# Kernel tuning notes

Measured on AMD Instinct MI355X. Metric: run time of the kernel, lower is better.

The kernel has to match this reference:

```python
import jax, jax.numpy as jnp
import numpy as np

NT, NTRACES, NCH = 4096, 1024, 4


def setup_inputs() -> dict:
    key = jax.random.key(0)
    k1, k2 = jax.random.split(key)
    x = jax.random.normal(k1, (NT, NTRACES, NCH), dtype=jnp.float32)
    y = jax.random.normal(k2, (NT, NTRACES, NCH), dtype=jnp.float32)
    return {"x": x, "y": y}


def _quantiles(qs, cws, values):
    # quantile function of the discrete measure (values, weights with cumsum cws)
    # evaluated at cumulative-mass levels qs (POT solver_1d convention:
    # searchsorted side='left', clipped to valid index range).
    idx = jnp.clip(jnp.searchsorted(cws, qs, side="left"), 0, values.shape[0] - 1)
    return values[idx]


def _emd2_1d(xv, yv, w):
    # 1D EMD^2 (sqeuclidean ground metric, as in ot.emd2_1d defaults) between
    # atoms at positions xv with weights w and atoms at yv with weights w.
    ix = jnp.argsort(xv)
    iy = jnp.argsort(yv)
    xs, ys = xv[ix], yv[iy]            # sorted positions
    ca = jnp.cumsum(w[ix])             # cumulative source mass
    cb = jnp.cumsum(w[iy])             # cumulative target mass (equal total)
    qs = jnp.sort(jnp.concatenate([ca, cb]))  # merged mass breakpoints, (2*nt,)
    qx = _quantiles(qs, ca, xs)
    qy = _quantiles(qs, cb, ys)
    delta = jnp.diff(qs, prepend=0.0)  # mass in each segment
    return jnp.sum(delta * (qx - qy) ** 2)


def _sinkhorn_pair(xv, yv, t):
    # faithful to Sinkhorn._sinkhorn: clamp(min=0) -> cumsum -> divide by the
    # SUM of the cumsum (note: not the last element) -> 1D EMD with positions
    # (xv, yv) and weights t = arange(nt)  [positional args of ot.emd2_1d].
    xv = jnp.cumsum(jnp.clip(xv, 0.0))
    yv = jnp.cumsum(jnp.clip(yv, 0.0))
    xv = xv / jnp.sum(xv)
    yv = yv / jnp.sum(yv)
    return _emd2_1d(xv, yv, t)


def reference(x, y):
    nt = x.shape[0]
    t = jnp.arange(nt, dtype=jnp.float32)
    xf = x.reshape(nt, -1).T  # (ntraces*nchannels, nt)
    yf = y.reshape(nt, -1).T
    losses = jax.vmap(_sinkhorn_pair, in_axes=(0, 0, None))(xf, yf, t)
    return jnp.sum(losses)
```

## Files before the change

### kernel.cpp

```cpp
#include <hip/hip_runtime.h>


#define NT   4096
#define NP   4096
#define CH   64
#define LCH  64
#define BLK  256

__global__ __launch_bounds__(BLK) void k1_chunk_sums(
    const float* __restrict__ x, const float* __restrict__ y,
    float* __restrict__ ax, float* __restrict__ ay,
    float* __restrict__ wx, float* __restrict__ wy) {
  const int p  = blockIdx.x * BLK + threadIdx.x;
  const int j  = blockIdx.y;
  const int t0 = j * LCH;
  const float* xp = x + (size_t)t0 * NP + p;
  const float* yp = y + (size_t)t0 * NP + p;
  float a_x = 0.f, a_y = 0.f, w_x = 0.f, w_y = 0.f;
#pragma unroll 8
  for (int i = 0; i < LCH; ++i) {
    float xv = fmaxf(xp[(size_t)i * NP], 0.f);
    float yv = fmaxf(yp[(size_t)i * NP], 0.f);
    const float wgt = (float)(NT - (t0 + i));
    a_x += xv;        a_y += yv;
    w_x += wgt * xv;  w_y += wgt * yv;
  }
  const int o = j * NP + p;
  ax[o] = a_x; ay[o] = a_y; wx[o] = w_x; wy[o] = w_y;
}

__global__ __launch_bounds__(BLK) void k2_scan(
    const float* __restrict__ ax, const float* __restrict__ ay,
    const float* __restrict__ wx, const float* __restrict__ wy,
    double* __restrict__ Ox, double* __restrict__ Oy,
    double* __restrict__ iSx, double* __restrict__ iSy) {
  const int p = blockIdx.x * BLK + threadIdx.x;
  double ox = 0.0, oy = 0.0, sx = 0.0, sy = 0.0;
  for (int j = 0; j < CH; ++j) {
    const int o = j * NP + p;
    Ox[o] = ox; Oy[o] = oy;
    ox += (double)ax[o]; oy += (double)ay[o];
    sx += (double)wx[o]; sy += (double)wy[o];
  }
  iSx[p] = 1.0 / sx;
  iSy[p] = 1.0 / sy;
}

__global__ __launch_bounds__(BLK) void k3_loss(
    const float* __restrict__ x, const float* __restrict__ y,
    const double* __restrict__ Ox, const double* __restrict__ Oy,
    const double* __restrict__ iSx, const double* __restrict__ iSy,
    double* __restrict__ part) {
  const int p  = blockIdx.x * BLK + threadIdx.x;
  const int j  = blockIdx.y;
  const int t0 = j * LCH;
  const float* xp = x + (size_t)t0 * NP + p;
  const float* yp = y + (size_t)t0 * NP + p;
  const int o = j * NP + p;
  double cx = Ox[o], cy = Oy[o];
  const double isx = iSx[p], isy = iSy[p];
  double acc = 0.0;
#pragma unroll 4
  for (int i = 0; i < LCH; ++i) {
    float xv = fmaxf(xp[(size_t)i * NP], 0.f);
    float yv = fmaxf(yp[(size_t)i * NP], 0.f);
    cx += (double)xv;
    cy += (double)yv;
    const double d = cx * isx - cy * isy;
    acc += (double)(t0 + i) * d * d;
  }
  __shared__ double red[BLK];
  red[threadIdx.x] = acc;
  __syncthreads();
  for (int s = BLK / 2; s > 0; s >>= 1) {
    if (threadIdx.x < s) red[threadIdx.x] += red[threadIdx.x + s];
    __syncthreads();
  }
  if (threadIdx.x == 0)
    part[blockIdx.y * gridDim.x + blockIdx.x] = red[0];
}

__global__ __launch_bounds__(1024) void k4_final(
    const double* __restrict__ part, float* __restrict__ out) {
  __shared__ double red[1024];
  red[threadIdx.x] = part[threadIdx.x];
  __syncthreads();
  for (int s = 512; s > 0; s >>= 1) {
    if (threadIdx.x < s) red[threadIdx.x] += red[threadIdx.x + s];
    __syncthreads();
  }
  if (threadIdx.x == 0) out[0] = (float)red[0];
}

extern "C" void kernel_launch(void* const* d_in, const int* in_sizes, int n_in,
                              void* d_out, int out_size, void* d_ws, size_t ws_size,
                              hipStream_t stream) {
  const float* x = (const float*)d_in[0];
  const float* y = (const float*)d_in[1];
  float* out = (float*)d_out;

  const size_t CNP = (size_t)CH * NP;
  char* ws = (char*)d_ws;
  float*  ax   = (float*)ws;            ws += CNP * sizeof(float);
  float*  ay   = (float*)ws;            ws += CNP * sizeof(float);
  float*  wx   = (float*)ws;            ws += CNP * sizeof(float);
  float*  wy   = (float*)ws;            ws += CNP * sizeof(float);
  double* Ox   = (double*)ws;           ws += CNP * sizeof(double);
  double* Oy   = (double*)ws;           ws += CNP * sizeof(double);
  double* iSx  = (double*)ws;           ws += (size_t)NP * sizeof(double);
  double* iSy  = (double*)ws;           ws += (size_t)NP * sizeof(double);
  double* part = (double*)ws;           ws += (size_t)(NP / BLK) * CH * sizeof(double);

  dim3 g1(NP / BLK, CH);
  k1_chunk_sums<<<g1, BLK, 0, stream>>>(x, y, ax, ay, wx, wy);
  k2_scan<<<NP / BLK, BLK, 0, stream>>>(ax, ay, wx, wy, Ox, Oy, iSx, iSy);
  k3_loss<<<g1, BLK, 0, stream>>>(x, y, Ox, Oy, iSx, iSy, part);
  k4_final<<<1, 1024, 0, stream>>>(part, out);
}
```

Baseline: 175.3 us.

## Expand squared loss into per-chunk moments to read inputs once

Instead of reading x and y twice (once for chunk sums, once for the loss pass), the first kernel computes per-chunk polynomial moments of the local cumsums (sums of t·c, t·c², t·cx·cy, etc.). A second kernel combines them algebraically with the chunk offsets and normalizers to get the loss, and the launches drop from four to three. This removes a full 128MB input reread but adds double-precision work per element and writes nine float arrays. Storing the moments as float may cost precision, and each thread now handles two columns via float2 loads.

```diff
diff --git a/kernel.cpp b/kernel.cpp
--- a/kernel.cpp
+++ b/kernel.cpp
@@ -6,90 +6,118 @@
 #define CH   64
 #define LCH  64
 #define BLK  256
+#define BLK2 64
 
-__global__ __launch_bounds__(BLK) void k1_chunk_sums(
+__global__ __launch_bounds__(BLK) void p1_moments(
     const float* __restrict__ x, const float* __restrict__ y,
-    float* __restrict__ ax, float* __restrict__ ay,
-    float* __restrict__ wx, float* __restrict__ wy) {
-  const int p  = blockIdx.x * BLK + threadIdx.x;
+    float* __restrict__ aX, float* __restrict__ aY,
+    float* __restrict__ uL, float* __restrict__ uM,
+    float* __restrict__ pL, float* __restrict__ pM,
+    float* __restrict__ pLL, float* __restrict__ pMM,
+    float* __restrict__ pLM)
+{
+  const int pv = blockIdx.x * BLK + threadIdx.x;
+  const int p0 = pv * 2;
   const int j  = blockIdx.y;
   const int t0 = j * LCH;
-  const float* xp = x + (size_t)t0 * NP + p;
-  const float* yp = y + (size_t)t0 * NP + p;
-  float a_x = 0.f, a_y = 0.f, w_x = 0.f, w_y = 0.f;
+  const float* xb = x + (size_t)t0 * NP + p0;
+  const float* yb = y + (size_t)t0 * NP + p0;
+
+  double cx0 = 0, cx1 = 0, cy0 = 0, cy1 = 0;
+  double uL0 = 0, uL1 = 0, uM0 = 0, uM1 = 0;
+  double pL0 = 0, pL1 = 0, pM0 = 0, pM1 = 0;
+  double pLL0 = 0, pLL1 = 0, pMM0 = 0, pMM1 = 0, pLM0 = 0, pLM1 = 0;
+
 #pragma unroll 8
   for (int i = 0; i < LCH; ++i) {
-    float xv = fmaxf(xp[(size_t)i * NP], 0.f);
-    float yv = fmaxf(yp[(size_t)i * NP], 0.f);
-    const float wgt = (float)(NT - (t0 + i));
-    a_x += xv;        a_y += yv;
-    w_x += wgt * xv;  w_y += wgt * yv;
+    const float2 xv = *(const float2*)(xb + (size_t)i * NP);
+    const float2 yv = *(const float2*)(yb + (size_t)i * NP);
+    const double td = (double)(t0 + i);
+
+    const double lx0 = (double)fmaxf(xv.x, 0.f);
+    const double lx1 = (double)fmaxf(xv.y, 0.f);
+    const double ly0 = (double)fmaxf(yv.x, 0.f);
+    const double ly1 = (double)fmaxf(yv.y, 0.f);
+
+    cx0 += lx0; cy0 += ly0;
+    const double tl0 = td * cx0;
+    const double tm0 = td * cy0;
+    pL0  += tl0;        pM0  += tm0;
+    pLL0 += tl0 * cx0;  pMM0 += tm0 * cy0;
+    pLM0 += tl0 * cy0;
+    uL0  += cx0;        uM0  += cy0;
+
+    cx1 += lx1; cy1 += ly1;
+    const double tl1 = td * cx1;
+    const double tm1 = td * cy1;
+    pL1  += tl1;        pM1  += tm1;
+    pLL1 += tl1 * cx1;  pMM1 += tm1 * cy1;
+    pLM1 += tl1 * cy1;
+    uL1  += cx1;        uM1  += cy1;
   }
-  const int o = j * NP + p;
-  ax[o] = a_x; ay[o] = a_y; wx[o] = w_x; wy[o] = w_y;
+
+  const size_t o = (size_t)j * NP + p0;
+  aX[o]  = (float)cx0;  aX[o+1]  = (float)cx1;
+  aY[o]  = (float)cy0;  aY[o+1]  = (float)cy1;
+  uL[o]  = (float)uL0;  uL[o+1]  = (float)uL1;
+  uM[o]  = (float)uM0;  uM[o+1]  = (float)uM1;
+  pL[o]  = (float)pL0;  pL[o+1]  = (float)pL1;
+  pM[o]  = (float)pM0;  pM[o+1]  = (float)pM1;
+  pLL[o] = (float)pLL0; pLL[o+1] = (float)pLL1;
+  pMM[o] = (float)pMM0; pMM[o+1] = (float)pMM1;
+  pLM[o] = (float)pLM0; pLM[o+1] = (float)pLM1;
 }
 
-__global__ __launch_bounds__(BLK) void k2_scan(
-    const float* __restrict__ ax, const float* __restrict__ ay,
-    const float* __restrict__ wx, const float* __restrict__ wy,
-    double* __restrict__ Ox, double* __restrict__ Oy,
-    double* __restrict__ iSx, double* __restrict__ iSy) {
-  const int p = blockIdx.x * BLK + threadIdx.x;
-  double ox = 0.0, oy = 0.0, sx = 0.0, sy = 0.0;
+__global__ __launch_bounds__(BLK2) void p2_loss(
+    const float* __restrict__ aX, const float* __restrict__ aY,
+    const float* __restrict__ uL, const float* __restrict__ uM,
+    const float* __restrict__ pL, const float* __restrict__ pM,
+    const float* __restrict__ pLL, const float* __restrict__ pMM,
+    const float* __restrict__ pLM,
+    double* __restrict__ part)
+{
+  const int p = blockIdx.x * BLK2 + threadIdx.x;
+
+  double O = 0, P = 0, Sx = 0, Sy = 0;
+#pragma unroll 8
   for (int j = 0; j < CH; ++j) {
-    const int o = j * NP + p;
-    Ox[o] = ox; Oy[o] = oy;
-    ox += (double)ax[o]; oy += (double)ay[o];
-    sx += (double)wx[o]; sy += (double)wy[o];
+    const size_t o = (size_t)j * NP + p;
+    Sx += (double)LCH * O + (double)uL[o];
+    Sy += (double)LCH * P + (double)uM[o];
+    O  += (double)aX[o];
+    P  += (double)aY[o];
   }
-  iSx[p] = 1.0 / sx;
-  iSy[p] = 1.0 / sy;
+  const double isx = 1.0 / Sx;
+  const double isy = 1.0 / Sy;
+
+  O = 0; P = 0;
+  double loss = 0;
+#pragma unroll 4
+  for (int j = 0; j < CH; ++j) {
+    const size_t o = (size_t)j * NP + p;
+    const double g  = isx * O - isy * P;
+    const double Tj = 4096.0 * (double)j + 2016.0;
+    const double sh  = isx * (double)pL[o] - isy * (double)pM[o];
+    const double shh = isx * isx * (double)pLL[o]
+                     - 2.0 * isx * isy * (double)pLM[o]
+                     + isy * isy * (double)pMM[o];
+    loss += g * g * Tj + 2.0 * g * sh + shh;
+    O += (double)aX[o];
+    P += (double)aY[o];
+  }
+
+  for (int s = 32; s > 0; s >>= 1)
+    loss += __shfl_down(loss, s, 64);
+  if (threadIdx.x == 0) part[blockIdx.x] = loss;
 }
 
-__global__ __launch_bounds__(BLK) void k3_loss(
-    const float* __restrict__ x, const float* __restrict__ y,
-    const double* __restrict__ Ox, const double* __restrict__ Oy,
-    const double* __restrict__ iSx, const double* __restrict__ iSy,
-    double* __restrict__ part) {
-  const int p  = blockIdx.x * BLK + threadIdx.x;
-  const int j  = blockIdx.y;
-  const int t0 = j * LCH;
-  const float* xp = x + (size_t)t0 * NP + p;
-  const float* yp = y + (size_t)t0 * NP + p;
-  const int o = j * NP + p;
-  double cx = Ox[o], cy = Oy[o];
-  const double isx = iSx[p], isy = iSy[p];
-  double acc = 0.0;
-#pragma unroll 4
-  for (int i = 0; i < LCH; ++i) {
-    float xv = fmaxf(xp[(size_t)i * NP], 0.f);
-    float yv = fmaxf(yp[(size_t)i * NP], 0.f);
-    cx += (double)xv;
-    cy += (double)yv;
-    const double d = cx * isx - cy * isy;
-    acc += (double)(t0 + i) * d * d;
-  }
-  __shared__ double red[BLK];
-  red[threadIdx.x] = acc;
-  __syncthreads();
-  for (int s = BLK / 2; s > 0; s >>= 1) {
-    if (threadIdx.x < s) red[threadIdx.x] += red[threadIdx.x + s];
-    __syncthreads();
-  }
-  if (threadIdx.x == 0)
-    part[blockIdx.y * gridDim.x + blockIdx.x] = red[0];
-}
-
-__global__ __launch_bounds__(1024) void k4_final(
-    const double* __restrict__ part, float* __restrict__ out) {
-  __shared__ double red[1024];
-  red[threadIdx.x] = part[threadIdx.x];
-  __syncthreads();
-  for (int s = 512; s > 0; s >>= 1) {
-    if (threadIdx.x < s) red[threadIdx.x] += red[threadIdx.x + s];
-    __syncthreads();
-  }
-  if (threadIdx.x == 0) out[0] = (float)red[0];
+__global__ __launch_bounds__(BLK2) void p3_final(
+    const double* __restrict__ part, float* __restrict__ out)
+{
+  double v = part[threadIdx.x];
+  for (int s = 32; s > 0; s >>= 1)
+    v += __shfl_down(v, s, 64);
+  if (threadIdx.x == 0) out[0] = (float)v;
 }
 
 extern "C" void kernel_launch(void* const* d_in, const int* in_sizes, int n_in,
@@ -101,19 +129,19 @@
 
   const size_t CNP = (size_t)CH * NP;
   char* ws = (char*)d_ws;
-  float*  ax   = (float*)ws;            ws += CNP * sizeof(float);
-  float*  ay   = (float*)ws;            ws += CNP * sizeof(float);
-  float*  wx   = (float*)ws;            ws += CNP * sizeof(float);
-  float*  wy   = (float*)ws;            ws += CNP * sizeof(float);
-  double* Ox   = (double*)ws;           ws += CNP * sizeof(double);
-  double* Oy   = (double*)ws;           ws += CNP * sizeof(double);
-  double* iSx  = (double*)ws;           ws += (size_t)NP * sizeof(double);
-  double* iSy  = (double*)ws;           ws += (size_t)NP * sizeof(double);
-  double* part = (double*)ws;           ws += (size_t)(NP / BLK) * CH * sizeof(double);
+  float* aX  = (float*)ws; ws += CNP * sizeof(float);
+  float* aY  = (float*)ws; ws += CNP * sizeof(float);
+  float* uL  = (float*)ws; ws += CNP * sizeof(float);
+  float* uM  = (float*)ws; ws += CNP * sizeof(float);
+  float* pL  = (float*)ws; ws += CNP * sizeof(float);
+  float* pM  = (float*)ws; ws += CNP * sizeof(float);
+  float* pLL = (float*)ws; ws += CNP * sizeof(float);
+  float* pMM = (float*)ws; ws += CNP * sizeof(float);
+  float* pLM = (float*)ws; ws += CNP * sizeof(float);
+  double* part = (double*)ws; ws += (size_t)(NP / BLK2) * sizeof(double);
 
-  dim3 g1(NP / BLK, CH);
-  k1_chunk_sums<<<g1, BLK, 0, stream>>>(x, y, ax, ay, wx, wy);
-  k2_scan<<<NP / BLK, BLK, 0, stream>>>(ax, ay, wx, wy, Ox, Oy, iSx, iSy);
-  k3_loss<<<g1, BLK, 0, stream>>>(x, y, Ox, Oy, iSx, iSy, part);
-  k4_final<<<1, 1024, 0, stream>>>(part, out);
+  dim3 g1((NP / 2) / BLK, CH);
+  p1_moments<<<g1, BLK, 0, stream>>>(x, y, aX, aY, uL, uM, pL, pM, pLL, pMM, pLM);
+  p2_loss<<<NP / BLK2, BLK2, 0, stream>>>(aX, aY, uL, uM, pL, pM, pLL, pMM, pLM, part);
+  p3_final<<<1, BLK2, 0, stream>>>(part, out);
 }
```

Measured after the change: 308.4 us. 1.76x slower.
